# Kernel tuning notes

Hardware: AMD Instinct MI355X
Metric: run time of the kernel (lower is better)

## Reference

```python
import jax, jax.numpy as jnp
import numpy as np
import math

D_MODEL = 2048
NUM_HEADS = 16
D_K = D_MODEL // NUM_HEADS  # 128
THETA = 10000.0
BATCH = 2
SEQ = 2048


def setup_inputs() -> dict:
    key = jax.random.key(0)
    k1, k2, k3 = jax.random.split(key, 3)
    std_qkv = math.sqrt(2.0 / (D_MODEL + 3 * D_MODEL))
    std_o = math.sqrt(2.0 / (D_MODEL + D_MODEL))
    return {
        "x": jax.random.normal(k1, (BATCH, SEQ, D_MODEL), dtype=jnp.float32),
        "token_positions": jnp.arange(SEQ, dtype=jnp.int64 if jax.config.jax_enable_x64 else jnp.int32),
        "Wqkv": jax.random.normal(k2, (3 * D_MODEL, D_MODEL), dtype=jnp.float32) * std_qkv,
        "Wo": jax.random.normal(k3, (D_MODEL, D_MODEL), dtype=jnp.float32) * std_o,
    }


def _rope(x, positions):
    # x: [b, h, t, d_k]; interleaved even/odd rotation as in the torch module
    half = D_K // 2
    inv_freq = 1.0 / (THETA ** (jnp.arange(half, dtype=x.dtype) / half))
    ang = positions.astype(x.dtype)[:, None] * inv_freq[None, :]  # [t, half]
    sin, cos = jnp.sin(ang), jnp.cos(ang)                          # broadcast over b,h
    x_even, x_odd = x[..., 0::2], x[..., 1::2]
    rot_even = x_even * cos - x_odd * sin
    rot_odd = x_even * sin + x_odd * cos
    return jnp.stack([rot_even, rot_odd], axis=-1).reshape(x.shape)


def reference(x, token_positions, Wqkv, Wo):
    B, T, _ = x.shape
    qkv = x @ Wqkv.T                                  # [b, t, 3*d_model]
    q, k, v = jnp.split(qkv, 3, axis=-1)
    def to_heads(t):
        return t.reshape(B, T, NUM_HEADS, D_K).transpose(0, 2, 1, 3)  # b h t d
    q, k, v = to_heads(q), to_heads(k), to_heads(v)
    q = _rope(q, token_positions)
    k = _rope(k, token_positions)
    scale = 1.0 / math.sqrt(D_K)
    scores = jnp.einsum("bhqd,bhkd->bhqk", q, k) * scale
    causal = jnp.tril(jnp.ones((T, T), dtype=bool))
    scores = jnp.where(causal, scores, jnp.finfo(scores.dtype).min)
    attn = jax.nn.softmax(scores, axis=-1)
    out = jnp.einsum("bhqk,bhkd->bhqd", attn, v)
    out = out.transpose(0, 2, 1, 3).reshape(B, T, D_MODEL)
    return out @ Wo.T
```

## Files before the change

### kernel.cpp

```cpp
#include <hip/hip_runtime.h>
#include <math.h>
#include <stdint.h>

#define NHEADS 16
#define DK 128
#define TSEQ 2048
#define DMODEL 2048

typedef __attribute__((ext_vector_type(8))) short short8;
typedef __attribute__((ext_vector_type(4))) float floatx4;

__device__ __forceinline__ float bf2f(unsigned short h) {
    return __uint_as_float(((unsigned int)h) << 16);
}
__device__ __forceinline__ unsigned short f2bf(float f) {
    unsigned int u = __float_as_uint(f);
    u += 0x7FFFu + ((u >> 16) & 1u);
    return (unsigned short)(u >> 16);
}
__device__ __forceinline__ void async16(unsigned short* lds, const unsigned short* g) {
    __builtin_amdgcn_global_load_lds(
        (const __attribute__((address_space(1))) uint32_t*)g,
        (__attribute__((address_space(3))) uint32_t*)lds, 16, 0, 0);
}

#define NX8 1048576
#define NW8 1572864
#define NO8 524288
__global__ __launch_bounds__(256) void cast_all_bf16(
    const float* __restrict__ x, const float* __restrict__ wqkv, const float* __restrict__ wo,
    unsigned short* __restrict__ xb, unsigned short* __restrict__ wqkvb, unsigned short* __restrict__ wob)
{
    const int i = blockIdx.x * 256 + threadIdx.x;
    const float* src; unsigned short* dst; int k;
    if (i < NX8)            { src = x;    dst = xb;    k = i; }
    else if (i < NX8 + NW8) { src = wqkv; dst = wqkvb; k = i - NX8; }
    else                    { src = wo;   dst = wob;   k = i - NX8 - NW8; }
    const float4* p4 = reinterpret_cast<const float4*>(src) + 2 * (size_t)k;
    const float4 a = p4[0], b = p4[1];
    uint32_t w0 = (uint32_t)f2bf(a.x) | ((uint32_t)f2bf(a.y) << 16);
    uint32_t w1 = (uint32_t)f2bf(a.z) | ((uint32_t)f2bf(a.w) << 16);
    uint32_t w2 = (uint32_t)f2bf(b.x) | ((uint32_t)f2bf(b.y) << 16);
    uint32_t w3 = (uint32_t)f2bf(b.z) | ((uint32_t)f2bf(b.w) << 16);
    uint4 o; o.x = w0; o.y = w1; o.z = w2; o.w = w3;
    *reinterpret_cast<uint4*>(dst + 8 * (size_t)k) = o;
}

__global__ __launch_bounds__(256) void rope_table_kernel(
    const int* __restrict__ pos, float2* __restrict__ tab)
{
    const int idx = blockIdx.x * 256 + threadIdx.x;
    const int tt = idx >> 6, i = idx & 63;
    const double inv_freq = exp(-log(10000.0) * (double)i / 64.0);
    const double ang = (double)pos[tt] * inv_freq;
    tab[idx] = make_float2((float)cos(ang), (float)sin(ang));
}

__global__ __launch_bounds__(256, 2) void gemm_qkv_x(
    const unsigned short* __restrict__ A, const unsigned short* __restrict__ B,
    unsigned short* __restrict__ qkvb, unsigned short* __restrict__ vt,
    const float2* __restrict__ tab)
{
    const int K = DMODEL, N = 3 * DMODEL;
    __shared__ unsigned short As[2][128 * 64];
    __shared__ unsigned short Bs[2][192 * 64];

    const int t = threadIdx.x;
    const int lane = t & 63, w = t >> 6;
    const int wr = w >> 1, wc = w & 1;
    const int lr = lane & 15, hi = lane >> 4;

    const int bid = (int)blockIdx.x;
    const int xcd = bid & 7, local = bid >> 3;
    const int row0 = (local & 31) * 128;
    const int col0 = ((xcd << 2) | (local >> 5)) * 192;

    const int rr = t >> 3;
    const int cc = ((t & 7) ^ (rr & 7)) << 3;
    const unsigned short* aP = A + (size_t)(row0 + rr) * K + cc;
    const unsigned short* bP = B + (size_t)(col0 + rr) * K + cc;
    const size_t rstep = (size_t)32 * K;

    floatx4 acc[4][6];
#pragma unroll
    for (int m = 0; m < 4; m++)
#pragma unroll
        for (int n = 0; n < 6; n++)
#pragma unroll
            for (int e = 0; e < 4; e++) acc[m][n][e] = 0.f;

#define STAGE(nb, k0n) do { \
        async16(&As[nb][t * 8],          aP + (k0n)); \
        async16(&As[nb][(t + 256) * 8],  aP + rstep + (k0n)); \
        async16(&As[nb][(t + 512) * 8],  aP + 2 * rstep + (k0n)); \
        async16(&As[nb][(t + 768) * 8],  aP + 3 * rstep + (k0n)); \
        async16(&Bs[nb][t * 8],          bP + (k0n)); \
        async16(&Bs[nb][(t + 256) * 8],  bP + rstep + (k0n)); \
        async16(&Bs[nb][(t + 512) * 8],  bP + 2 * rstep + (k0n)); \
        async16(&Bs[nb][(t + 768) * 8],  bP + 3 * rstep + (k0n)); \
        async16(&Bs[nb][(t + 1024) * 8], bP + 4 * rstep + (k0n)); \
        async16(&Bs[nb][(t + 1280) * 8], bP + 5 * rstep + (k0n)); \
    } while (0)

    const int NT = K >> 6;
    const int ch0 = (hi ^ (lr & 7)) * 8;
    const int ch1 = ((4 + hi) ^ (lr & 7)) * 8;

    short8 av[4], bv[6];

#define RD_AV(Ac, ch) do { \
        _Pragma("unroll") \
        for (int m = 0; m < 4; m++) \
            av[m] = *(const short8*)&(Ac)[(wr * 64 + m * 16 + lr) * 64 + (ch)]; \
    } while (0)
#define RD_BV(Bc, ch) do { \
        _Pragma("unroll") \
        for (int n = 0; n < 6; n++) \
            bv[n] = *(const short8*)&(Bc)[(wc * 96 + n * 16 + lr) * 64 + (ch)]; \
    } while (0)
#define MFMA_ALL() do { \
        _Pragma("unroll") \
        for (int m = 0; m < 4; m++) \
            _Pragma("unroll") \
            for (int n = 0; n < 6; n++) \
                acc[m][n] = __builtin_amdgcn_mfma_f32_16x16x32_bf16(av[m], bv[n], acc[m][n], 0, 0, 0); \
    } while (0)

    STAGE(0, 0);

    for (int kt = 0; kt < NT; ++kt) {
        const int cur = kt & 1;
        const unsigned short* __restrict__ Ac = &As[cur][0];
        const unsigned short* __restrict__ Bc = &Bs[cur][0];
        const bool more = (kt + 1 < NT);

        if (more) {
            STAGE(cur ^ 1, (kt + 1) << 6);
            asm volatile("s_waitcnt vmcnt(10)" ::: "memory");
        } else {
            asm volatile("s_waitcnt vmcnt(0)" ::: "memory");
        }
        __builtin_amdgcn_s_barrier();

        RD_AV(Ac, ch0); RD_BV(Bc, ch0);
        asm volatile("s_waitcnt lgkmcnt(0)" ::: "memory");
        __builtin_amdgcn_sched_barrier(0);
        __builtin_amdgcn_s_setprio(1);
        MFMA_ALL();
        __builtin_amdgcn_s_setprio(0);

        RD_AV(Ac, ch1); RD_BV(Bc, ch1);
        asm volatile("s_waitcnt lgkmcnt(0)" ::: "memory");
        __builtin_amdgcn_sched_barrier(0);
        __builtin_amdgcn_s_setprio(1);
        MFMA_ALL();
        __builtin_amdgcn_s_setprio(0);

        __builtin_amdgcn_s_barrier();
    }
#undef STAGE
#undef RD_AV
#undef RD_BV
#undef MFMA_ALL

    const int par = lr & 1;
#pragma unroll
    for (int mi = 0; mi < 4; mi++) {
        const int row = row0 + wr * 64 + mi * 16 + hi * 4;
        const int tt = row & (TSEQ - 1);
        const int bb = row >> 11;
#pragma unroll
        for (int ni = 0; ni < 6; ni++) {
            const int col = col0 + wc * 96 + ni * 16 + lr;
            if (col < 2 * DMODEL) {
                const int pi = (col & 127) >> 1;
#pragma unroll
                for (int j = 0; j < 4; j++) {
                    const float2 cs = tab[(tt + j) * 64 + pi];
                    const float v = acc[mi][ni][j];
                    const float p = __shfl_xor(v, 1, 64);
                    const float o = par ? (p * cs.y + v * cs.x)
                                        : (v * cs.x - p * cs.y);
                    qkvb[(size_t)(row + j) * N + col] = f2bf(o);
                }
            } else {
                const int vcol = col - 2 * DMODEL;
                const int h = vcol >> 7, d = vcol & 127;
                uint2 pw;
                pw.x = (uint32_t)f2bf(acc[mi][ni][0]) | ((uint32_t)f2bf(acc[mi][ni][1]) << 16);
                pw.y = (uint32_t)f2bf(acc[mi][ni][2]) | ((uint32_t)f2bf(acc[mi][ni][3]) << 16);
                *(uint2*)&vt[(size_t)((bb * NHEADS + h) * DK + d) * TSEQ + tt] = pw;
            }
        }
    }
}

__global__ __launch_bounds__(256, 2) void gemm_o_x(
    const unsigned short* __restrict__ A, const unsigned short* __restrict__ B,
    float* __restrict__ C)
{
    const int K = DMODEL, N = DMODEL;
    __shared__ unsigned short As[2][128 * 64];
    __shared__ unsigned short Bs[2][128 * 64];

    const int t = threadIdx.x;
    const int lane = t & 63, w = t >> 6;
    const int wr = w >> 1, wc = w & 1;
    const int lr = lane & 15, hi = lane >> 4;

    const int bid = (int)blockIdx.x;
    const int xcd = bid & 7, local = bid >> 3;
    const int row0 = (local & 31) * 128;
    const int col0 = ((xcd << 1) | (local >> 5)) * 128;

    const int rr = t >> 3;
    const int cc = ((t & 7) ^ (rr & 7)) << 3;
    const unsigned short* aP = A + (size_t)(row0 + rr) * K + cc;
    const unsigned short* bP = B + (size_t)(col0 + rr) * K + cc;
    const size_t rstep = (size_t)32 * K;

    floatx4 acc[4][4];
#pragma unroll
    for (int m = 0; m < 4; m++)
#pragma unroll
        for (int n = 0; n < 4; n++)
#pragma unroll
            for (int e = 0; e < 4; e++) acc[m][n][e] = 0.f;

#define STAGE(nb, k0n) do { \
        async16(&As[nb][t * 8],          aP + (k0n)); \
        async16(&As[nb][(t + 256) * 8],  aP + rstep + (k0n)); \
        async16(&As[nb][(t + 512) * 8],  aP + 2 * rstep + (k0n)); \
        async16(&As[nb][(t + 768) * 8],  aP + 3 * rstep + (k0n)); \
        async16(&Bs[nb][t * 8],          bP + (k0n)); \
        async16(&Bs[nb][(t + 256) * 8],  bP + rstep + (k0n)); \
        async16(&Bs[nb][(t + 512) * 8],  bP + 2 * rstep + (k0n)); \
        async16(&Bs[nb][(t + 768) * 8],  bP + 3 * rstep + (k0n)); \
    } while (0)

    const int NT = K >> 6;
    const int ch0 = (hi ^ (lr & 7)) * 8;
    const int ch1 = ((4 + hi) ^ (lr & 7)) * 8;

    short8 av[4], bv[4];

#define RD_AV(Ac, ch) do { \
        _Pragma("unroll") \
        for (int m = 0; m < 4; m++) \
            av[m] = *(const short8*)&(Ac)[(wr * 64 + m * 16 + lr) * 64 + (ch)]; \
    } while (0)
#define RD_BV(Bc, ch) do { \
        _Pragma("unroll") \
        for (int n = 0; n < 4; n++) \
            bv[n] = *(const short8*)&(Bc)[(wc * 64 + n * 16 + lr) * 64 + (ch)]; \
    } while (0)
#define MFMA_ALL() do { \
        _Pragma("unroll") \
        for (int m = 0; m < 4; m++) \
            _Pragma("unroll") \
            for (int n = 0; n < 4; n++) \
                acc[m][n] = __builtin_amdgcn_mfma_f32_16x16x32_bf16(av[m], bv[n], acc[m][n], 0, 0, 0); \
    } while (0)

    STAGE(0, 0);

    for (int kt = 0; kt < NT; ++kt) {
        const int cur = kt & 1;
        const unsigned short* __restrict__ Ac = &As[cur][0];
        const unsigned short* __restrict__ Bc = &Bs[cur][0];
        const bool more = (kt + 1 < NT);

        if (more) {
            STAGE(cur ^ 1, (kt + 1) << 6);
            asm volatile("s_waitcnt vmcnt(8)" ::: "memory");
        } else {
            asm volatile("s_waitcnt vmcnt(0)" ::: "memory");
        }
        __builtin_amdgcn_s_barrier();

        RD_AV(Ac, ch0); RD_BV(Bc, ch0);
        asm volatile("s_waitcnt lgkmcnt(0)" ::: "memory");
        __builtin_amdgcn_sched_barrier(0);
        __builtin_amdgcn_s_setprio(1);
        MFMA_ALL();
        __builtin_amdgcn_s_setprio(0);

        RD_AV(Ac, ch1); RD_BV(Bc, ch1);
        asm volatile("s_waitcnt lgkmcnt(0)" ::: "memory");
        __builtin_amdgcn_sched_barrier(0);
        __builtin_amdgcn_s_setprio(1);
        MFMA_ALL();
        __builtin_amdgcn_s_setprio(0);

        __builtin_amdgcn_s_barrier();
    }
#undef STAGE
#undef RD_AV
#undef RD_BV
#undef MFMA_ALL

#pragma unroll
    for (int mi = 0; mi < 4; mi++) {
        const int row = row0 + wr * 64 + mi * 16 + hi * 4;
#pragma unroll
        for (int ni = 0; ni < 4; ni++) {
            const int col = col0 + wc * 64 + ni * 16 + lr;
#pragma unroll
            for (int j = 0; j < 4; j++)
                C[(size_t)(row + j) * N + col] = acc[mi][ni][j];
        }
    }
}

__global__ __launch_bounds__(512, 1) void attn_mfma3_kernel(
    const unsigned short* __restrict__ qkvb, const unsigned short* __restrict__ vt,
    unsigned short* __restrict__ outb)
{
    __shared__ unsigned short Ks[2][64 * 128];
    __shared__ unsigned short Vs[128 * 64];
    __shared__ unsigned short Ps[8][32 * 64];

    const int t = threadIdx.x;
    const int lane = t & 63, w = t >> 6;
    const int lr = lane & 15, hi = lane >> 4;
    const int bh = (int)blockIdx.x >> 3;
    const int p  = (int)blockIdx.x & 7;
    const int b = bh >> 4, h = bh & 15;
    const int chunk = (w < 4) ? p : (15 - p);
    const int q0w = chunk * 128 + (w & 3) * 32;
    const float scale = 0.08838834764831845f;
    const size_t QROW = 3 * DMODEL;

    const unsigned short* kg = qkvb + (size_t)b * TSEQ * QROW + DMODEL + h * DK;
    const unsigned short* vg = vt + (size_t)bh * DK * TSEQ;

    short8 qf[2][4];
    {
        const unsigned short* qbase = qkvb + (size_t)(b * TSEQ + q0w) * QROW + h * DK;
#pragma unroll
        for (int nt = 0; nt < 2; nt++)
#pragma unroll
            for (int ks = 0; ks < 4; ks++) {
                short8 raw = *(const short8*)(qbase + (size_t)(nt * 16 + lr) * QROW + ks * 32 + hi * 8);
                short8 sc;
#pragma unroll
                for (int e = 0; e < 8; e++)
                    sc[e] = (short)f2bf(bf2f((unsigned short)raw[e]) * scale);
                qf[nt][ks] = sc;
            }
    }

    auto stageK = [&](int bufi, int kv0s) {
#pragma unroll
        for (int i = 0; i < 2; i++) {
            const int s = i * 512 + t;
            const int r = s >> 4;
            const int cc = (s & 15) ^ (r & 7);
            async16(&Ks[bufi][s * 8], kg + (size_t)(kv0s + r) * QROW + cc * 8);
        }
    };
    auto stageV = [&](int kv0s) {
#pragma unroll
        for (int i = 0; i < 2; i++) {
            const int s = i * 512 + t;
            const int r = s >> 3;
            const int cc = (s & 7) ^ (r & 7);
            async16(&Vs[s * 8], vg + (size_t)r * TSEQ + kv0s + cc * 8);
        }
    };

    floatx4 accO[2][8];
#pragma unroll
    for (int nt = 0; nt < 2; nt++)
#pragma unroll
        for (int dt = 0; dt < 8; dt++)
#pragma unroll
            for (int e = 0; e < 4; e++) accO[nt][dt][e] = 0.f;
    float mrun[2] = {-1e30f, -1e30f};
    float lrun[2] = {0.f, 0.f};

    const int ntiles = (15 - p) * 2 + 2;
    int kbuf = 0;

    stageK(0, 0);
    __syncthreads();

    const int pswz = (lr & 7) << 1;

    for (int ti = 0; ti < ntiles; ti++) {
        const int kv0 = ti * 64;
        const bool havK = (ti + 1 < ntiles);
        stageV(kv0);
        if (havK) stageK(kbuf ^ 1, kv0 + 64);

        const bool active = (kv0 <= q0w + 31);
        float al[2] = {1.f, 1.f};

        if (active) {
            floatx4 st[4][2];
#pragma unroll
            for (int mt = 0; mt < 4; mt++)
#pragma unroll
                for (int nt = 0; nt < 2; nt++)
#pragma unroll
                    for (int e = 0; e < 4; e++) st[mt][nt][e] = 0.f;
#pragma unroll
            for (int mt = 0; mt < 4; mt++) {
                const int r = mt * 16 + lr;
#pragma unroll
                for (int ks = 0; ks < 4; ks++) {
                    const int ch = (ks * 4 + hi) ^ (r & 7);
                    const short8 kf = *(const short8*)&Ks[kbuf][(r * 16 + ch) * 8];
                    st[mt][0] = __builtin_amdgcn_mfma_f32_16x16x32_bf16(kf, qf[0][ks], st[mt][0], 0, 0, 0);
                    st[mt][1] = __builtin_amdgcn_mfma_f32_16x16x32_bf16(kf, qf[1][ks], st[mt][1], 0, 0, 0);
                }
            }
            if (kv0 + 63 > q0w) {
#pragma unroll
                for (int nt = 0; nt < 2; nt++) {
                    const int qg = q0w + nt * 16 + lr;
#pragma unroll
                    for (int mt = 0; mt < 4; mt++)
#pragma unroll
                        for (int rg = 0; rg < 4; rg++) {
                            const int kvg = kv0 + mt * 16 + hi * 4 + rg;
                            if (kvg > qg) st[mt][nt][rg] = -1e30f;
                        }
                }
            }
            float pm[2];
#pragma unroll
            for (int nt = 0; nt < 2; nt++) {
                float m = -1e30f;
#pragma unroll
                for (int mt = 0; mt < 4; mt++)
#pragma unroll
                    for (int rg = 0; rg < 4; rg++) m = fmaxf(m, st[mt][nt][rg]);
                m = fmaxf(m, __shfl_xor(m, 16, 64));
                m = fmaxf(m, __shfl_xor(m, 32, 64));
                pm[nt] = m;
            }
            if (__any((pm[0] > mrun[0] + 8.f) || (pm[1] > mrun[1] + 8.f))) {
#pragma unroll
                for (int nt = 0; nt < 2; nt++) {
                    const float mn = fmaxf(mrun[nt], pm[nt]);
                    al[nt] = __expf(mrun[nt] - mn);
                    mrun[nt] = mn;
                }
#pragma unroll
                for (int rg = 0; rg < 4; rg++) {
                    const float a0 = __shfl(al[0], hi * 4 + rg, 64);
                    const float a1 = __shfl(al[1], hi * 4 + rg, 64);
#pragma unroll
                    for (int dt = 0; dt < 8; dt++) {
                        accO[0][dt][rg] *= a0;
                        accO[1][dt][rg] *= a1;
                    }
                }
            }
#pragma unroll
            for (int nt = 0; nt < 2; nt++) {
                float ls = 0.f;
                const int prow = nt * 16 + lr;
#pragma unroll
                for (int mt = 0; mt < 4; mt++) {
                    float pv[4];
#pragma unroll
                    for (int rg = 0; rg < 4; rg++) {
                        pv[rg] = __expf(st[mt][nt][rg] - mrun[nt]);
                        ls += pv[rg];
                    }
                    uint2 pw;
                    pw.x = (uint32_t)f2bf(pv[0]) | ((uint32_t)f2bf(pv[1]) << 16);
                    pw.y = (uint32_t)f2bf(pv[2]) | ((uint32_t)f2bf(pv[3]) << 16);
                    const int chunkx = (mt * 4 + hi) ^ pswz;
                    *(uint2*)&Ps[w][prow * 64 + chunkx * 4] = pw;
                }
                ls += __shfl_xor(ls, 16, 64);
                ls += __shfl_xor(ls, 32, 64);
                lrun[nt] = lrun[nt] * al[nt] + ls;
            }
        }
        if (havK) asm volatile("s_waitcnt vmcnt(2)" ::: "memory");
        else      asm volatile("s_waitcnt vmcnt(0)" ::: "memory");
        __builtin_amdgcn_s_barrier();

        if (active) {
#pragma unroll
            for (int ks2 = 0; ks2 < 2; ks2++) {
                const int ch0 = ((ks2 * 8 + hi * 2) ^ pswz) * 4;
                const short8 pa0 = *(const short8*)&Ps[w][(0 * 16 + lr) * 64 + ch0];
                const short8 pa1 = *(const short8*)&Ps[w][(1 * 16 + lr) * 64 + ch0];
#pragma unroll
                for (int dt = 0; dt < 8; dt++) {
                    const int r = dt * 16 + lr;
                    const int ch = (ks2 * 4 + hi) ^ (r & 7);
                    const short8 vf = *(const short8*)&Vs[(r * 8 + ch) * 8];
                    accO[0][dt] = __builtin_amdgcn_mfma_f32_16x16x32_bf16(pa0, vf, accO[0][dt], 0, 0, 0);
                    accO[1][dt] = __builtin_amdgcn_mfma_f32_16x16x32_bf16(pa1, vf, accO[1][dt], 0, 0, 0);
                }
            }
        }
        asm volatile("s_waitcnt vmcnt(0)" ::: "memory");
        __builtin_amdgcn_s_barrier();
        kbuf ^= 1;
    }

#pragma unroll
    for (int nt = 0; nt < 2; nt++) {
        const float lv_own = 1.f / lrun[nt];
#pragma unroll
        for (int rg = 0; rg < 4; rg++) {
            const float lv = __shfl(lv_own, hi * 4 + rg, 64);
            unsigned short* orow = outb + (size_t)(b * TSEQ + q0w + nt * 16 + hi * 4 + rg) * DMODEL + h * DK;
#pragma unroll
            for (int dt = 0; dt < 8; dt++)
                orow[dt * 16 + lr] = f2bf(accO[nt][dt][rg] * lv);
        }
    }
}

extern "C" void kernel_launch(void* const* d_in, const int* in_sizes, int n_in,
                              void* d_out, int out_size, void* d_ws, size_t ws_size,
                              hipStream_t stream)
{
    const float* x    = (const float*)d_in[0];
    const int*   pos  = (const int*)d_in[1];
    const float* Wqkv = (const float*)d_in[2];
    const float* Wo   = (const float*)d_in[3];
    float* out = (float*)d_out;

    unsigned short* qkvb  = (unsigned short*)d_ws;
    unsigned short* vtb   = qkvb + (size_t)25165824;
    unsigned short* xb    = vtb + (size_t)8388608;
    unsigned short* attnb = xb;
    unsigned short* wqkvb = xb + (size_t)8388608;
    unsigned short* wob   = wqkvb + (size_t)12582912;
    float2* tab = (float2*)(wob + (size_t)4194304);

    cast_all_bf16<<<12288, 256, 0, stream>>>(x, Wqkv, Wo, xb, wqkvb, wob);
    rope_table_kernel<<<512, 256, 0, stream>>>(pos, tab);

    gemm_qkv_x<<<dim3(1024), 256, 0, stream>>>(xb, wqkvb, qkvb, vtb, tab);

    attn_mfma3_kernel<<<dim3(256), 512, 0, stream>>>(qkvb, vtb, attnb);

    gemm_o_x<<<dim3(512), 256, 0, stream>>>(attnb, wob, out);
}
```

Baseline: 260.2 us.

## Double-buffer V tiles and drop mid-iteration barrier in attention kernel

The attention kernel now double-buffers V alongside K, prefetching the next K and V tiles one iteration ahead. This removes the mid-iteration wait and barrier between the softmax and the PV product, leaving one barrier per tile. Block index mapping is also changed so consecutive blocks share the same work chunk across different batch-heads, which evens out load across the grid. The cost is extra LDS for the second V buffer; with launch bounds of one block per CU this should be affordable.

```diff
diff --git a/kernel.cpp b/kernel.cpp
--- a/kernel.cpp
+++ b/kernel.cpp
@@ -312,19 +312,19 @@
     }
 }
 
-__global__ __launch_bounds__(512, 1) void attn_mfma3_kernel(
+__global__ __launch_bounds__(512, 1) void attn_mfma4_kernel(
     const unsigned short* __restrict__ qkvb, const unsigned short* __restrict__ vt,
     unsigned short* __restrict__ outb)
 {
     __shared__ unsigned short Ks[2][64 * 128];
-    __shared__ unsigned short Vs[128 * 64];
+    __shared__ unsigned short Vs[2][128 * 64];
     __shared__ unsigned short Ps[8][32 * 64];
 
     const int t = threadIdx.x;
     const int lane = t & 63, w = t >> 6;
     const int lr = lane & 15, hi = lane >> 4;
-    const int bh = (int)blockIdx.x >> 3;
-    const int p  = (int)blockIdx.x & 7;
+    const int bh = (int)blockIdx.x & 31;
+    const int p  = (int)blockIdx.x >> 5;
     const int b = bh >> 4, h = bh & 15;
     const int chunk = (w < 4) ? p : (15 - p);
     const int q0w = chunk * 128 + (w & 3) * 32;
@@ -359,13 +359,13 @@
             async16(&Ks[bufi][s * 8], kg + (size_t)(kv0s + r) * QROW + cc * 8);
         }
     };
-    auto stageV = [&](int kv0s) {
+    auto stageV = [&](int bufi, int kv0s) {
 #pragma unroll
         for (int i = 0; i < 2; i++) {
             const int s = i * 512 + t;
             const int r = s >> 3;
             const int cc = (s & 7) ^ (r & 7);
-            async16(&Vs[s * 8], vg + (size_t)r * TSEQ + kv0s + cc * 8);
+            async16(&Vs[bufi][s * 8], vg + (size_t)r * TSEQ + kv0s + cc * 8);
         }
     };
 
@@ -379,24 +379,27 @@
     float mrun[2] = {-1e30f, -1e30f};
     float lrun[2] = {0.f, 0.f};
 
-    const int ntiles = (15 - p) * 2 + 2;
-    int kbuf = 0;
+    const int ntiles = (16 - p) * 2;
+    int buf = 0;
 
     stageK(0, 0);
-    __syncthreads();
+    stageV(0, 0);
+    asm volatile("s_waitcnt vmcnt(0)" ::: "memory");
+    __builtin_amdgcn_s_barrier();
 
     const int pswz = (lr & 7) << 1;
 
     for (int ti = 0; ti < ntiles; ti++) {
         const int kv0 = ti * 64;
-        const bool havK = (ti + 1 < ntiles);
-        stageV(kv0);
-        if (havK) stageK(kbuf ^ 1, kv0 + 64);
+        if (ti + 1 < ntiles) {
+            stageK(buf ^ 1, kv0 + 64);
+            stageV(buf ^ 1, kv0 + 64);
+        }
 
         const bool active = (kv0 <= q0w + 31);
-        float al[2] = {1.f, 1.f};
 
         if (active) {
+            float al[2] = {1.f, 1.f};
             floatx4 st[4][2];
 #pragma unroll
             for (int mt = 0; mt < 4; mt++)
@@ -410,7 +413,7 @@
 #pragma unroll
                 for (int ks = 0; ks < 4; ks++) {
                     const int ch = (ks * 4 + hi) ^ (r & 7);
-                    const short8 kf = *(const short8*)&Ks[kbuf][(r * 16 + ch) * 8];
+                    const short8 kf = *(const short8*)&Ks[buf][(r * 16 + ch) * 8];
                     st[mt][0] = __builtin_amdgcn_mfma_f32_16x16x32_bf16(kf, qf[0][ks], st[mt][0], 0, 0, 0);
                     st[mt][1] = __builtin_amdgcn_mfma_f32_16x16x32_bf16(kf, qf[1][ks], st[mt][1], 0, 0, 0);
                 }
@@ -480,30 +483,26 @@
                 ls += __shfl_xor(ls, 32, 64);
                 lrun[nt] = lrun[nt] * al[nt] + ls;
             }
-        }
-        if (havK) asm volatile("s_waitcnt vmcnt(2)" ::: "memory");
-        else      asm volatile("s_waitcnt vmcnt(0)" ::: "memory");
-        __builtin_amdgcn_s_barrier();
-
-        if (active) {
+
 #pragma unroll
             for (int ks2 = 0; ks2 < 2; ks2++) {
-                const int ch0 = ((ks2 * 8 + hi * 2) ^ pswz) * 4;
-                const short8 pa0 = *(const short8*)&Ps[w][(0 * 16 + lr) * 64 + ch0];
-                const short8 pa1 = *(const short8*)&Ps[w][(1 * 16 + lr) * 64 + ch0];
+                const int chp = ((ks2 * 8 + hi * 2) ^ pswz) * 4;
+                const short8 pa0 = *(const short8*)&Ps[w][(0 * 16 + lr) * 64 + chp];
+                const short8 pa1 = *(const short8*)&Ps[w][(1 * 16 + lr) * 64 + chp];
 #pragma unroll
                 for (int dt = 0; dt < 8; dt++) {
                     const int r = dt * 16 + lr;
                     const int ch = (ks2 * 4 + hi) ^ (r & 7);
-                    const short8 vf = *(const short8*)&Vs[(r * 8 + ch) * 8];
+                    const short8 vf = *(const short8*)&Vs[buf][(r * 8 + ch) * 8];
                     accO[0][dt] = __builtin_amdgcn_mfma_f32_16x16x32_bf16(pa0, vf, accO[0][dt], 0, 0, 0);
                     accO[1][dt] = __builtin_amdgcn_mfma_f32_16x16x32_bf16(pa1, vf, accO[1][dt], 0, 0, 0);
                 }
             }
         }
+
         asm volatile("s_waitcnt vmcnt(0)" ::: "memory");
         __builtin_amdgcn_s_barrier();
-        kbuf ^= 1;
+        buf ^= 1;
     }
 
 #pragma unroll
@@ -543,7 +542,7 @@
 
     gemm_qkv_x<<<dim3(1024), 256, 0, stream>>>(xb, wqkvb, qkvb, vtb, tab);
 
-    attn_mfma3_kernel<<<dim3(256), 512, 0, stream>>>(qkvb, vtb, attnb);
+    attn_mfma4_kernel<<<dim3(256), 512, 0, stream>>>(qkvb, vtb, attnb);
 
     gemm_o_x<<<dim3(512), 256, 0, stream>>>(attnb, wob, out);
 }
```

After: 256.8 us. About the same (-1.3%).
